# Kernel tuning notes

Hardware: AMD Instinct MI355X
Metric: run time of the kernel (lower is better)

The kernel has to match this reference:

```python
import jax, jax.numpy as jnp
import numpy as np

E = 768
H_HEADS = 12


def trilinear_border_sample(feat_map, coords):
    """grid_sample 3D, mode='bilinear', padding_mode='border', align_corners=True.
    feat_map: (B, C, D, H, W); coords: (B, P, 3) in [-1,1], last dim = (x, y, z) -> (W, H, D).
    Returns (B, P, C).
    """
    B, C, D, H, W = feat_map.shape
    x, y, z = coords[..., 0], coords[..., 1], coords[..., 2]
    ix = (x + 1.0) * 0.5 * (W - 1)
    iy = (y + 1.0) * 0.5 * (H - 1)
    iz = (z + 1.0) * 0.5 * (D - 1)
    x0 = jnp.floor(ix); y0 = jnp.floor(iy); z0 = jnp.floor(iz)
    wx = ix - x0; wy = iy - y0; wz = iz - z0
    x0i = jnp.clip(x0, 0, W - 1).astype(jnp.int32)
    x1i = jnp.clip(x0 + 1, 0, W - 1).astype(jnp.int32)
    y0i = jnp.clip(y0, 0, H - 1).astype(jnp.int32)
    y1i = jnp.clip(y0 + 1, 0, H - 1).astype(jnp.int32)
    z0i = jnp.clip(z0, 0, D - 1).astype(jnp.int32)
    z1i = jnp.clip(z0 + 1, 0, D - 1).astype(jnp.int32)
    flat = feat_map.reshape(B, C, D * H * W)

    def gather(zi, yi, xi):
        idx = (zi * H + yi) * W + xi  # (B, P)
        return jnp.take_along_axis(flat, idx[:, None, :], axis=2)  # (B, C, P)

    out = (
        gather(z0i, y0i, x0i) * ((1 - wz) * (1 - wy) * (1 - wx))[:, None, :]
        + gather(z0i, y0i, x1i) * ((1 - wz) * (1 - wy) * wx)[:, None, :]
        + gather(z0i, y1i, x0i) * ((1 - wz) * wy * (1 - wx))[:, None, :]
        + gather(z0i, y1i, x1i) * ((1 - wz) * wy * wx)[:, None, :]
        + gather(z1i, y0i, x0i) * (wz * (1 - wy) * (1 - wx))[:, None, :]
        + gather(z1i, y0i, x1i) * (wz * (1 - wy) * wx)[:, None, :]
        + gather(z1i, y1i, x0i) * (wz * wy * (1 - wx))[:, None, :]
        + gather(z1i, y1i, x1i) * (wz * wy * wx)[:, None, :]
    )
    return out.transpose(0, 2, 1)  # (B, P, C)


def setup_inputs() -> dict:
    key = jax.random.key(0)
    ks = jax.random.split(key, 12)
    B, fullN, nb = 64, 513, 32
    s = 1.0 / np.sqrt(E)
    return {
        "x": jax.random.normal(ks[0], (B, fullN, E), jnp.float32),
        "bio_embed": jax.random.normal(ks[1], (B, E), jnp.float32),
        "base_coords": jax.random.uniform(ks[2], (nb, 3), jnp.float32),
        "offsets": jax.random.normal(ks[3], (B, nb, 3), jnp.float32) * 0.1,
        "confidence": jax.random.uniform(ks[4], (B, 1), jnp.float32),
        "sample_proj_w": jax.random.uniform(ks[5], (E, E), jnp.float32, -s, s),
        "sample_proj_b": jax.random.uniform(ks[6], (E,), jnp.float32, -s, s),
        "in_proj_w": jax.random.uniform(ks[7], (3 * E, E), jnp.float32, -s, s),
        "in_proj_b": jnp.zeros((3 * E,), jnp.float32),
        "out_proj_w": jax.random.uniform(ks[8], (E, E), jnp.float32, -s, s),
        "out_proj_b": jnp.zeros((E,), jnp.float32),
        "grid_size": 8,
    }


def reference(x, bio_embed, base_coords, offsets, confidence,
              sample_proj_w, sample_proj_b, in_proj_w, in_proj_b,
              out_proj_w, out_proj_b, grid_size):
    B, fullN, C = x.shape
    G = grid_size
    patch_tokens = x[:, 1:, :]  # (B, N, C), N = G^3
    feat_map = patch_tokens.transpose(0, 2, 1).reshape(B, C, G, G, G)

    coords = jnp.clip(base_coords[None, :, :] + offsets, -1.0, 1.0)  # (B, nb, 3)
    sampled = trilinear_border_sample(feat_map, coords)  # (B, nb, C)
    sampled = sampled @ sample_proj_w.T + sample_proj_b

    # MultiheadAttention: single query (bio_embed), keys/values = sampled tokens
    hd = E // H_HEADS
    Wq, Wk, Wv = in_proj_w[:E], in_proj_w[E:2 * E], in_proj_w[2 * E:]
    bq, bk, bv = in_proj_b[:E], in_proj_b[E:2 * E], in_proj_b[2 * E:]
    q = (bio_embed @ Wq.T + bq).reshape(B, H_HEADS, hd)
    k = (sampled @ Wk.T + bk).reshape(B, -1, H_HEADS, hd)
    v = (sampled @ Wv.T + bv).reshape(B, -1, H_HEADS, hd)
    scores = jnp.einsum('bhd,bphd->bhp', q, k) / jnp.sqrt(jnp.asarray(hd, q.dtype))
    attn = jax.nn.softmax(scores, axis=-1)
    ctx = jnp.einsum('bhp,bphd->bhd', attn, v).reshape(B, E)
    attn_out = ctx @ out_proj_w.T + out_proj_b  # (B, E)

    out = jnp.broadcast_to(attn_out[:, None, :], (B, fullN, C))
    out = out * confidence[:, :, None]
    return out
```

## Files before the change

### kernel.cpp

```cpp
#include <hip/hip_runtime.h>
#include <hip/hip_bf16.h>
#include <math.h>

#define E 768
#define NH 12
#define HD 64

typedef __attribute__((ext_vector_type(8))) short bf16x8;
typedef __attribute__((ext_vector_type(4))) float f32x4;

__device__ __forceinline__ unsigned short f2bf_rne(float f) {
    unsigned int u = __float_as_uint(f);
    u += 0x7FFF + ((u >> 16) & 1);
    return (unsigned short)(u >> 16);
}

__global__ void conv_bf16(const float* __restrict__ src,
                          unsigned short* __restrict__ dst, int n)
{
    int i = blockIdx.x * blockDim.x + threadIdx.x;
    if (i < n) dst[i] = f2bf_rne(src[i]);
}

__global__ void sample_kernel(const float* __restrict__ x,
                              const float* __restrict__ base_coords,
                              const float* __restrict__ offsets,
                              const int* __restrict__ gsize,
                              unsigned short* __restrict__ sampled,
                              int B, int P, int fullN)
{
    int bp = blockIdx.x;
    int b = bp / P, p = bp % P;
    int G = *gsize;
    float gm1 = (float)(G - 1);

    float cx = base_coords[p * 3 + 0] + offsets[bp * 3 + 0];
    float cy = base_coords[p * 3 + 1] + offsets[bp * 3 + 1];
    float cz = base_coords[p * 3 + 2] + offsets[bp * 3 + 2];
    cx = fminf(fmaxf(cx, -1.f), 1.f);
    cy = fminf(fmaxf(cy, -1.f), 1.f);
    cz = fminf(fmaxf(cz, -1.f), 1.f);

    float ix = (cx + 1.f) * 0.5f * gm1;
    float iy = (cy + 1.f) * 0.5f * gm1;
    float iz = (cz + 1.f) * 0.5f * gm1;
    float fx = floorf(ix), fy = floorf(iy), fz = floorf(iz);
    float wx = ix - fx, wy = iy - fy, wz = iz - fz;

    int x0 = (int)fminf(fmaxf(fx,       0.f), gm1);
    int x1 = (int)fminf(fmaxf(fx + 1.f, 0.f), gm1);
    int y0 = (int)fminf(fmaxf(fy,       0.f), gm1);
    int y1 = (int)fminf(fmaxf(fy + 1.f, 0.f), gm1);
    int z0 = (int)fminf(fmaxf(fz,       0.f), gm1);
    int z1 = (int)fminf(fmaxf(fz + 1.f, 0.f), gm1);

    int t000 = (z0 * G + y0) * G + x0;
    int t001 = (z0 * G + y0) * G + x1;
    int t010 = (z0 * G + y1) * G + x0;
    int t011 = (z0 * G + y1) * G + x1;
    int t100 = (z1 * G + y0) * G + x0;
    int t101 = (z1 * G + y0) * G + x1;
    int t110 = (z1 * G + y1) * G + x0;
    int t111 = (z1 * G + y1) * G + x1;

    float w000 = (1.f - wz) * (1.f - wy) * (1.f - wx);
    float w001 = (1.f - wz) * (1.f - wy) * wx;
    float w010 = (1.f - wz) * wy * (1.f - wx);
    float w011 = (1.f - wz) * wy * wx;
    float w100 = wz * (1.f - wy) * (1.f - wx);
    float w101 = wz * (1.f - wy) * wx;
    float w110 = wz * wy * (1.f - wx);
    float w111 = wz * wy * wx;

    const float* xb = x + ((size_t)b * fullN + 1) * E;
    unsigned short* outp = sampled + (size_t)bp * E;
    for (int c = threadIdx.x; c < E; c += blockDim.x) {
        float v = w000 * xb[(size_t)t000 * E + c]
                + w001 * xb[(size_t)t001 * E + c]
                + w010 * xb[(size_t)t010 * E + c]
                + w011 * xb[(size_t)t011 * E + c]
                + w100 * xb[(size_t)t100 * E + c]
                + w101 * xb[(size_t)t101 * E + c]
                + w110 * xb[(size_t)t110 * E + c]
                + w111 * xb[(size_t)t111 * E + c];
        outp[c] = f2bf_rne(v);
    }
}

template <bool OUT_BF16>
__global__ __launch_bounds__(256) void gemm_bf16_nt(
    const unsigned short* __restrict__ A,
    const unsigned short* __restrict__ W,
    const float* __restrict__ bias,
    void* __restrict__ C,
    int M, int N, int K)
{
    __shared__ unsigned short lsA[128 * 32];
    __shared__ unsigned short lsB[128 * 32];

    int wv = threadIdx.x >> 6;
    int ln = threadIdx.x & 63;
    int m0 = blockIdx.y * 128;
    int n0 = blockIdx.x * 128;
    int wm = (wv & 1) * 64;
    int wn = (wv >> 1) * 64;

    f32x4 acc[4][4] = {};

    int srow = ln >> 2;
    int scol = (ln & 3) * 8;

    for (int k0 = 0; k0 < K; k0 += 32) {
#pragma unroll
        for (int c = 0; c < 2; ++c) {
            int chunk = wv * 2 + c;
            int row = chunk * 16 + srow;
            const unsigned short* ga = A + (size_t)(m0 + row) * K + k0 + scol;
            const unsigned short* gw = W + (size_t)(n0 + row) * K + k0 + scol;
            __builtin_amdgcn_global_load_lds(
                (const __attribute__((address_space(1))) unsigned int*)ga,
                (__attribute__((address_space(3))) unsigned int*)(lsA + chunk * 16 * 32),
                16, 0, 0);
            __builtin_amdgcn_global_load_lds(
                (const __attribute__((address_space(1))) unsigned int*)gw,
                (__attribute__((address_space(3))) unsigned int*)(lsB + chunk * 16 * 32),
                16, 0, 0);
        }
        __syncthreads();

        int kq = (ln >> 4) * 8;
        int rsel = ln & 15;
        bf16x8 af[4], bfr[4];
#pragma unroll
        for (int i = 0; i < 4; ++i) {
            af[i]  = *(const bf16x8*)&lsA[(wm + i * 16 + rsel) * 32 + kq];
            bfr[i] = *(const bf16x8*)&lsB[(wn + i * 16 + rsel) * 32 + kq];
        }
#pragma unroll
        for (int i = 0; i < 4; ++i)
#pragma unroll
            for (int j = 0; j < 4; ++j)
                acc[i][j] = __builtin_amdgcn_mfma_f32_16x16x32_bf16(
                    af[i], bfr[j], acc[i][j], 0, 0, 0);
        __syncthreads();
    }

    int cr = (ln >> 4) * 4;
    int cc = ln & 15;
#pragma unroll
    for (int j = 0; j < 4; ++j) {
        int col = n0 + wn + j * 16 + cc;
        float bv = bias[col];
#pragma unroll
        for (int i = 0; i < 4; ++i) {
#pragma unroll
            for (int r = 0; r < 4; ++r) {
                int row = m0 + wm + i * 16 + cr + r;
                float v = acc[i][j][r] + bv;
                if (OUT_BF16)
                    ((unsigned short*)C)[(size_t)row * N + col] = f2bf_rne(v);
                else
                    ((float*)C)[(size_t)row * N + col] = v;
            }
        }
    }
}

__global__ void matvec_nt(const float* __restrict__ A,
                          const float* __restrict__ W,
                          const float* __restrict__ bias,
                          float* __restrict__ C,
                          int M, int N, int K)
{
    int wid = blockIdx.x * (blockDim.x >> 6) + (threadIdx.x >> 6);
    int ln = threadIdx.x & 63;
    if (wid >= M * N) return;
    int m = wid / N, n = wid % N;
    const float* a = A + (size_t)m * K;
    const float* w = W + (size_t)n * K;
    float s = 0.f;
    for (int k = ln; k < K; k += 64) s += a[k] * w[k];
#pragma unroll
    for (int off = 32; off; off >>= 1) s += __shfl_down(s, off);
    if (ln == 0) C[wid] = s + bias[n];
}

__global__ void attn_kernel(const float* __restrict__ q,
                            const float* __restrict__ kv,
                            float* __restrict__ ctx,
                            int B, int P)
{
    int bh = blockIdx.x;
    int b = bh / NH, h = bh % NH;
    int d = threadIdx.x;

    __shared__ float qs[HD];
    __shared__ float sc[64];

    qs[d] = q[(size_t)b * E + h * HD + d];
    __syncthreads();

    if (d < P) {
        const float* kr = kv + ((size_t)(b * P + d)) * (2 * E) + h * HD;
        float s = 0.f;
#pragma unroll
        for (int e = 0; e < HD; ++e) s += qs[e] * kr[e];
        sc[d] = s * 0.125f;
    }
    __syncthreads();

    float mx = -INFINITY;
    for (int p = 0; p < P; ++p) mx = fmaxf(mx, sc[p]);
    float den = 0.f;
    for (int p = 0; p < P; ++p) den += __expf(sc[p] - mx);
    __syncthreads();
    if (d < P) sc[d] = __expf(sc[d] - mx) / den;
    __syncthreads();

    float acc = 0.f;
    for (int p = 0; p < P; ++p)
        acc += sc[p] * kv[((size_t)(b * P + p)) * (2 * E) + E + h * HD + d];
    ctx[(size_t)b * E + h * HD + d] = acc;
}

__global__ void bcast_kernel(const float* __restrict__ attn_out,
                             const float* __restrict__ conf,
                             float* __restrict__ out,
                             int fullN, int pc)
{
    int b = blockIdx.y;
    float cf = conf[b];
    const float4* ao = (const float4*)(attn_out + (size_t)b * E);
    float4* ob = (float4*)(out + (size_t)b * fullN * E);
    int i = blockIdx.x * blockDim.x + threadIdx.x;
    if (i < pc) {
        int c4 = i % (E / 4);
        float4 v = ao[c4];
        v.x *= cf; v.y *= cf; v.z *= cf; v.w *= cf;
        ob[i] = v;
    }
}

extern "C" void kernel_launch(void* const* d_in, const int* in_sizes, int n_in,
                              void* d_out, int out_size, void* d_ws, size_t ws_size,
                              hipStream_t stream)
{
    const float* x      = (const float*)d_in[0];
    const float* bio    = (const float*)d_in[1];
    const float* bcrd   = (const float*)d_in[2];
    const float* offs   = (const float*)d_in[3];
    const float* conf   = (const float*)d_in[4];
    const float* spw    = (const float*)d_in[5];
    const float* spb    = (const float*)d_in[6];
    const float* ipw    = (const float*)d_in[7];
    const float* ipb    = (const float*)d_in[8];
    const float* opw    = (const float*)d_in[9];
    const float* opb    = (const float*)d_in[10];
    const int*   gsize  = (const int*)d_in[11];
    float* out = (float*)d_out;

    const int B     = in_sizes[1] / E;
    const int P     = in_sizes[2] / 3;
    const int fullN = in_sizes[0] / (B * E);
    const int M     = B * P;

    char* base = (char*)d_out;
    unsigned short* sampled_bf = (unsigned short*)(base + 0);
    unsigned short* sproj_bf   = (unsigned short*)(base + 3145728);
    unsigned short* spw_bf     = (unsigned short*)(base + 6291456);
    unsigned short* ipwkv_bf   = (unsigned short*)(base + 7471104);
    float*          kv         = (float*)(base + 9830400);
    float*          q          = (float*)(base + 22413312);
    float*          ctx        = (float*)(base + 22609920);
    float*          aout       = (float*)d_ws;

    int n_spw = E * E;
    int n_kvw = 2 * E * E;
    conv_bf16<<<(n_spw + 255) / 256, 256, 0, stream>>>(spw, spw_bf, n_spw);
    conv_bf16<<<(n_kvw + 255) / 256, 256, 0, stream>>>(ipw + (size_t)E * E, ipwkv_bf, n_kvw);

    sample_kernel<<<M, 256, 0, stream>>>(x, bcrd, offs, gsize, sampled_bf, B, P, fullN);

    gemm_bf16_nt<true><<<dim3(E / 128, M / 128), 256, 0, stream>>>(
        sampled_bf, spw_bf, spb, sproj_bf, M, E, E);

    gemm_bf16_nt<false><<<dim3(2 * E / 128, M / 128), 256, 0, stream>>>(
        sproj_bf, ipwkv_bf, ipb + E, kv, M, 2 * E, E);

    {
        int tot = B * E;
        matvec_nt<<<(tot + 3) / 4, 256, 0, stream>>>(bio, ipw, ipb, q, B, E, E);
    }

    attn_kernel<<<B * NH, 64, 0, stream>>>(q, kv, ctx, B, P);

    {
        int tot = B * E;
        matvec_nt<<<(tot + 3) / 4, 256, 0, stream>>>(ctx, opw, opb, aout, B, E, E);
    }

    int pc = fullN * E / 4;
    bcast_kernel<<<dim3((pc + 255) / 256, B), 256, 0, stream>>>(aout, conf, out, fullN, pc);
}
```

Baseline: 313.6 us.

## Fuse preprocessing kernels and merge attention with output projection

Weight bf16 conversions, trilinear sampling and the query matvec now run in one heterogeneous launch, with blocks dispatched by index range. Sampling and conversions use float4 loads. Attention, softmax and the output projection are merged into one kernel with one block per batch. This removes several launches and the ctx round trip to memory, but the fused out-proj matvec uses only B=64 blocks, each thread reading a full weight row serially, so parallelism drops compared with the earlier one-wave-per-output matvec.

```diff
diff --git a/kernel.cpp b/kernel.cpp
--- a/kernel.cpp
+++ b/kernel.cpp
@@ -15,75 +15,118 @@
     return (unsigned short)(u >> 16);
 }
 
-__global__ void conv_bf16(const float* __restrict__ src,
-                          unsigned short* __restrict__ dst, int n)
-{
-    int i = blockIdx.x * blockDim.x + threadIdx.x;
-    if (i < n) dst[i] = f2bf_rne(src[i]);
-}
-
-__global__ void sample_kernel(const float* __restrict__ x,
-                              const float* __restrict__ base_coords,
-                              const float* __restrict__ offsets,
-                              const int* __restrict__ gsize,
-                              unsigned short* __restrict__ sampled,
-                              int B, int P, int fullN)
-{
-    int bp = blockIdx.x;
-    int b = bp / P, p = bp % P;
-    int G = *gsize;
-    float gm1 = (float)(G - 1);
-
-    float cx = base_coords[p * 3 + 0] + offsets[bp * 3 + 0];
-    float cy = base_coords[p * 3 + 1] + offsets[bp * 3 + 1];
-    float cz = base_coords[p * 3 + 2] + offsets[bp * 3 + 2];
-    cx = fminf(fmaxf(cx, -1.f), 1.f);
-    cy = fminf(fmaxf(cy, -1.f), 1.f);
-    cz = fminf(fmaxf(cz, -1.f), 1.f);
-
-    float ix = (cx + 1.f) * 0.5f * gm1;
-    float iy = (cy + 1.f) * 0.5f * gm1;
-    float iz = (cz + 1.f) * 0.5f * gm1;
-    float fx = floorf(ix), fy = floorf(iy), fz = floorf(iz);
-    float wx = ix - fx, wy = iy - fy, wz = iz - fz;
-
-    int x0 = (int)fminf(fmaxf(fx,       0.f), gm1);
-    int x1 = (int)fminf(fmaxf(fx + 1.f, 0.f), gm1);
-    int y0 = (int)fminf(fmaxf(fy,       0.f), gm1);
-    int y1 = (int)fminf(fmaxf(fy + 1.f, 0.f), gm1);
-    int z0 = (int)fminf(fmaxf(fz,       0.f), gm1);
-    int z1 = (int)fminf(fmaxf(fz + 1.f, 0.f), gm1);
-
-    int t000 = (z0 * G + y0) * G + x0;
-    int t001 = (z0 * G + y0) * G + x1;
-    int t010 = (z0 * G + y1) * G + x0;
-    int t011 = (z0 * G + y1) * G + x1;
-    int t100 = (z1 * G + y0) * G + x0;
-    int t101 = (z1 * G + y0) * G + x1;
-    int t110 = (z1 * G + y1) * G + x0;
-    int t111 = (z1 * G + y1) * G + x1;
-
-    float w000 = (1.f - wz) * (1.f - wy) * (1.f - wx);
-    float w001 = (1.f - wz) * (1.f - wy) * wx;
-    float w010 = (1.f - wz) * wy * (1.f - wx);
-    float w011 = (1.f - wz) * wy * wx;
-    float w100 = wz * (1.f - wy) * (1.f - wx);
-    float w101 = wz * (1.f - wy) * wx;
-    float w110 = wz * wy * (1.f - wx);
-    float w111 = wz * wy * wx;
-
-    const float* xb = x + ((size_t)b * fullN + 1) * E;
-    unsigned short* outp = sampled + (size_t)bp * E;
-    for (int c = threadIdx.x; c < E; c += blockDim.x) {
-        float v = w000 * xb[(size_t)t000 * E + c]
-                + w001 * xb[(size_t)t001 * E + c]
-                + w010 * xb[(size_t)t010 * E + c]
-                + w011 * xb[(size_t)t011 * E + c]
-                + w100 * xb[(size_t)t100 * E + c]
-                + w101 * xb[(size_t)t101 * E + c]
-                + w110 * xb[(size_t)t110 * E + c]
-                + w111 * xb[(size_t)t111 * E + c];
-        outp[c] = f2bf_rne(v);
+__global__ __launch_bounds__(256) void fused_pre(
+    const float* __restrict__ spw, const float* __restrict__ ipw,
+    const float* __restrict__ ipb, const float* __restrict__ x,
+    const float* __restrict__ bcrd, const float* __restrict__ offs,
+    const int* __restrict__ gsize, const float* __restrict__ bio,
+    unsigned short* __restrict__ spw_bf, unsigned short* __restrict__ kvw_bf,
+    unsigned short* __restrict__ sampled, float* __restrict__ q,
+    int B, int P, int fullN,
+    int nb_conv1, int nb_conv2)
+{
+    __shared__ float sm[E];
+    int blk = blockIdx.x;
+    int t = threadIdx.x;
+
+    if (blk < nb_conv1) {
+        int i = blk * 256 + t;
+        float4 v = ((const float4*)spw)[i];
+        ushort4 o;
+        o.x = f2bf_rne(v.x); o.y = f2bf_rne(v.y);
+        o.z = f2bf_rne(v.z); o.w = f2bf_rne(v.w);
+        ((ushort4*)spw_bf)[i] = o;
+        return;
+    }
+    blk -= nb_conv1;
+    if (blk < nb_conv2) {
+        int i = blk * 256 + t;
+        float4 v = ((const float4*)(ipw + (size_t)E * E))[i];
+        ushort4 o;
+        o.x = f2bf_rne(v.x); o.y = f2bf_rne(v.y);
+        o.z = f2bf_rne(v.z); o.w = f2bf_rne(v.w);
+        ((ushort4*)kvw_bf)[i] = o;
+        return;
+    }
+    blk -= nb_conv2;
+    if (blk < B * P) {
+        int bp = blk;
+        int b = bp / P, p = bp % P;
+        int G = *gsize;
+        float gm1 = (float)(G - 1);
+
+        float cx = bcrd[p * 3 + 0] + offs[bp * 3 + 0];
+        float cy = bcrd[p * 3 + 1] + offs[bp * 3 + 1];
+        float cz = bcrd[p * 3 + 2] + offs[bp * 3 + 2];
+        cx = fminf(fmaxf(cx, -1.f), 1.f);
+        cy = fminf(fmaxf(cy, -1.f), 1.f);
+        cz = fminf(fmaxf(cz, -1.f), 1.f);
+
+        float ix = (cx + 1.f) * 0.5f * gm1;
+        float iy = (cy + 1.f) * 0.5f * gm1;
+        float iz = (cz + 1.f) * 0.5f * gm1;
+        float fx = floorf(ix), fy = floorf(iy), fz = floorf(iz);
+        float wx = ix - fx, wy = iy - fy, wz = iz - fz;
+
+        int x0 = (int)fminf(fmaxf(fx,       0.f), gm1);
+        int x1 = (int)fminf(fmaxf(fx + 1.f, 0.f), gm1);
+        int y0 = (int)fminf(fmaxf(fy,       0.f), gm1);
+        int y1 = (int)fminf(fmaxf(fy + 1.f, 0.f), gm1);
+        int z0 = (int)fminf(fmaxf(fz,       0.f), gm1);
+        int z1 = (int)fminf(fmaxf(fz + 1.f, 0.f), gm1);
+
+        int tk[8];
+        tk[0] = (z0 * G + y0) * G + x0;
+        tk[1] = (z0 * G + y0) * G + x1;
+        tk[2] = (z0 * G + y1) * G + x0;
+        tk[3] = (z0 * G + y1) * G + x1;
+        tk[4] = (z1 * G + y0) * G + x0;
+        tk[5] = (z1 * G + y0) * G + x1;
+        tk[6] = (z1 * G + y1) * G + x0;
+        tk[7] = (z1 * G + y1) * G + x1;
+        float wgt[8];
+        wgt[0] = (1.f - wz) * (1.f - wy) * (1.f - wx);
+        wgt[1] = (1.f - wz) * (1.f - wy) * wx;
+        wgt[2] = (1.f - wz) * wy * (1.f - wx);
+        wgt[3] = (1.f - wz) * wy * wx;
+        wgt[4] = wz * (1.f - wy) * (1.f - wx);
+        wgt[5] = wz * (1.f - wy) * wx;
+        wgt[6] = wz * wy * (1.f - wx);
+        wgt[7] = wz * wy * wx;
+
+        const float4* xb4 = (const float4*)(x + ((size_t)b * fullN + 1) * E);
+        ushort4* outp = (ushort4*)(sampled + (size_t)bp * E);
+        for (int c4 = t; c4 < E / 4; c4 += 256) {
+            float4 acc = {0.f, 0.f, 0.f, 0.f};
+#pragma unroll
+            for (int k = 0; k < 8; ++k) {
+                float4 v = xb4[(size_t)tk[k] * (E / 4) + c4];
+                acc.x += wgt[k] * v.x; acc.y += wgt[k] * v.y;
+                acc.z += wgt[k] * v.z; acc.w += wgt[k] * v.w;
+            }
+            ushort4 o;
+            o.x = f2bf_rne(acc.x); o.y = f2bf_rne(acc.y);
+            o.z = f2bf_rne(acc.z); o.w = f2bf_rne(acc.w);
+            outp[c4] = o;
+        }
+        return;
+    }
+    blk -= B * P;
+    {
+        int b = blk;
+        for (int c = t; c < E; c += 256) sm[c] = bio[(size_t)b * E + c];
+        __syncthreads();
+        for (int n = t; n < E; n += 256) {
+            const float4* w4 = (const float4*)(ipw + (size_t)n * E);
+            float s = 0.f;
+#pragma unroll 4
+            for (int k4 = 0; k4 < E / 4; ++k4) {
+                float4 w = w4[k4];
+                s += w.x * sm[k4 * 4] + w.y * sm[k4 * 4 + 1]
+                   + w.z * sm[k4 * 4 + 2] + w.w * sm[k4 * 4 + 3];
+            }
+            q[(size_t)b * E + n] = s + ipb[n];
+        }
     }
 }
 
@@ -166,61 +209,66 @@
     }
 }
 
-__global__ void matvec_nt(const float* __restrict__ A,
-                          const float* __restrict__ W,
-                          const float* __restrict__ bias,
-                          float* __restrict__ C,
-                          int M, int N, int K)
-{
-    int wid = blockIdx.x * (blockDim.x >> 6) + (threadIdx.x >> 6);
-    int ln = threadIdx.x & 63;
-    if (wid >= M * N) return;
-    int m = wid / N, n = wid % N;
-    const float* a = A + (size_t)m * K;
-    const float* w = W + (size_t)n * K;
-    float s = 0.f;
-    for (int k = ln; k < K; k += 64) s += a[k] * w[k];
-#pragma unroll
-    for (int off = 32; off; off >>= 1) s += __shfl_down(s, off);
-    if (ln == 0) C[wid] = s + bias[n];
-}
-
-__global__ void attn_kernel(const float* __restrict__ q,
-                            const float* __restrict__ kv,
-                            float* __restrict__ ctx,
-                            int B, int P)
-{
-    int bh = blockIdx.x;
-    int b = bh / NH, h = bh % NH;
-    int d = threadIdx.x;
-
-    __shared__ float qs[HD];
-    __shared__ float sc[64];
-
-    qs[d] = q[(size_t)b * E + h * HD + d];
+__global__ __launch_bounds__(256) void attn_out_kernel(
+    const float* __restrict__ q, const float* __restrict__ kv,
+    const float* __restrict__ opw, const float* __restrict__ opb,
+    float* __restrict__ aout, int P)
+{
+    int b = blockIdx.x;
+    int t = threadIdx.x;
+    __shared__ float qs[E];
+    __shared__ float aw[NH * 64];
+    __shared__ float cs[E];
+
+    for (int c = t; c < E; c += 256) qs[c] = q[(size_t)b * E + c];
     __syncthreads();
 
-    if (d < P) {
-        const float* kr = kv + ((size_t)(b * P + d)) * (2 * E) + h * HD;
+    for (int s = t; s < NH * P; s += 256) {
+        int h = s / P, p = s % P;
+        const float4* kr = (const float4*)(kv + ((size_t)(b * P + p)) * (2 * E) + h * HD);
+        const float* qh = qs + h * HD;
+        float acc = 0.f;
+#pragma unroll
+        for (int k4 = 0; k4 < HD / 4; ++k4) {
+            float4 kvv = kr[k4];
+            acc += kvv.x * qh[k4 * 4] + kvv.y * qh[k4 * 4 + 1]
+                 + kvv.z * qh[k4 * 4 + 2] + kvv.w * qh[k4 * 4 + 3];
+        }
+        aw[h * 64 + p] = acc * 0.125f;
+    }
+    __syncthreads();
+
+    if (t < NH) {
+        float mx = -INFINITY;
+        for (int p = 0; p < P; ++p) mx = fmaxf(mx, aw[t * 64 + p]);
+        float den = 0.f;
+        for (int p = 0; p < P; ++p) den += __expf(aw[t * 64 + p] - mx);
+        float inv = 1.f / den;
+        for (int p = 0; p < P; ++p) aw[t * 64 + p] = __expf(aw[t * 64 + p] - mx) * inv;
+    }
+    __syncthreads();
+
+    for (int c = t; c < E; c += 256) {
+        int h = c >> 6, d = c & 63;
+        const float* vbase = kv + E + h * HD + d;
+        float acc = 0.f;
+        for (int p = 0; p < P; ++p)
+            acc += aw[h * 64 + p] * vbase[((size_t)(b * P + p)) * (2 * E)];
+        cs[c] = acc;
+    }
+    __syncthreads();
+
+    for (int n = t; n < E; n += 256) {
+        const float4* w4 = (const float4*)(opw + (size_t)n * E);
         float s = 0.f;
-#pragma unroll
-        for (int e = 0; e < HD; ++e) s += qs[e] * kr[e];
-        sc[d] = s * 0.125f;
-    }
-    __syncthreads();
-
-    float mx = -INFINITY;
-    for (int p = 0; p < P; ++p) mx = fmaxf(mx, sc[p]);
-    float den = 0.f;
-    for (int p = 0; p < P; ++p) den += __expf(sc[p] - mx);
-    __syncthreads();
-    if (d < P) sc[d] = __expf(sc[d] - mx) / den;
-    __syncthreads();
-
-    float acc = 0.f;
-    for (int p = 0; p < P; ++p)
-        acc += sc[p] * kv[((size_t)(b * P + p)) * (2 * E) + E + h * HD + d];
-    ctx[(size_t)b * E + h * HD + d] = acc;
+#pragma unroll 4
+        for (int k4 = 0; k4 < E / 4; ++k4) {
+            float4 w = w4[k4];
+            s += w.x * cs[k4 * 4] + w.y * cs[k4 * 4 + 1]
+               + w.z * cs[k4 * 4 + 2] + w.w * cs[k4 * 4 + 3];
+        }
+        aout[(size_t)b * E + n] = s + opb[n];
+    }
 }
 
 __global__ void bcast_kernel(const float* __restrict__ attn_out,
@@ -271,15 +319,14 @@
     unsigned short* ipwkv_bf   = (unsigned short*)(base + 7471104);
     float*          kv         = (float*)(base + 9830400);
     float*          q          = (float*)(base + 22413312);
-    float*          ctx        = (float*)(base + 22609920);
     float*          aout       = (float*)d_ws;
 
-    int n_spw = E * E;
-    int n_kvw = 2 * E * E;
-    conv_bf16<<<(n_spw + 255) / 256, 256, 0, stream>>>(spw, spw_bf, n_spw);
-    conv_bf16<<<(n_kvw + 255) / 256, 256, 0, stream>>>(ipw + (size_t)E * E, ipwkv_bf, n_kvw);
-
-    sample_kernel<<<M, 256, 0, stream>>>(x, bcrd, offs, gsize, sampled_bf, B, P, fullN);
+    int nb_conv1 = (E * E) / 1024;
+    int nb_conv2 = (2 * E * E) / 1024;
+    int nblocks  = nb_conv1 + nb_conv2 + M + B;
+    fused_pre<<<nblocks, 256, 0, stream>>>(spw, ipw, ipb, x, bcrd, offs, gsize, bio,
+                                           spw_bf, ipwkv_bf, sampled_bf, q,
+                                           B, P, fullN, nb_conv1, nb_conv2);
 
     gemm_bf16_nt<true><<<dim3(E / 128, M / 128), 256, 0, stream>>>(
         sampled_bf, spw_bf, spb, sproj_bf, M, E, E);
@@ -287,17 +334,7 @@
     gemm_bf16_nt<false><<<dim3(2 * E / 128, M / 128), 256, 0, stream>>>(
         sproj_bf, ipwkv_bf, ipb + E, kv, M, 2 * E, E);
 
-    {
-        int tot = B * E;
-        matvec_nt<<<(tot + 3) / 4, 256, 0, stream>>>(bio, ipw, ipb, q, B, E, E);
-    }
-
-    attn_kernel<<<B * NH, 64, 0, stream>>>(q, kv, ctx, B, P);
-
-    {
-        int tot = B * E;
-        matvec_nt<<<(tot + 3) / 4, 256, 0, stream>>>(ctx, opw, opb, aout, B, E, E);
-    }
+    attn_out_kernel<<<B, 256, 0, stream>>>(q, kv, opw, opb, aout, P);
 
     int pc = fullN * E / 4;
     bcast_kernel<<<dim3((pc + 255) / 256, B), 256, 0, stream>>>(aout, conf, out, fullN, pc);
```

After: 447.7 us. 42.8% more time.
